# Performance work log

Measured on AMD Instinct MI355X. Metric: run time of the kernel, lower is better.

The kernel has to match this reference:

```python
import jax, jax.numpy as jnp
import numpy as np

ALPHA = 0.01
GAMMA = 4.0
SPATIAL_WEIGHT = 0.3
SEQ_LEN = 1024
LINE_WINDOW = 2


def setup_inputs() -> dict:
    key = jax.random.key(0)
    k1, k2, k3 = jax.random.split(key, 3)
    B, S, C = 64, SEQ_LEN, 8
    pred = jax.random.normal(k1, (B * S, C), dtype=jnp.float32)
    target = (jax.random.uniform(k2, (B * S, C)) < 0.05).astype(jnp.float32)
    # line indices: monotone non-decreasing within each sequence, ~256 lines
    lines = jnp.sort(
        jax.random.randint(k3, (B, S), 0, 256, dtype=jnp.int32), axis=-1
    ).reshape(-1)
    return {"pred": pred, "target": target, "token_to_line": lines}


def _spatial_penalty(pred, target, token_to_line):
    # pred/target: [B*S, C], token_to_line: [B*S]
    C = pred.shape[1]
    B = pred.shape[0] // SEQ_LEN if pred.shape[0] > SEQ_LEN else 1
    p = pred.reshape(B, SEQ_LEN, C)
    t = target.reshape(B, SEQ_LEN, C)
    l = token_to_line.reshape(B, SEQ_LEN)

    # nearby_mask[b,i,j] = |line_j - line_i| <= 2 and j != i
    diff = jnp.abs(l[:, :, None] - l[:, None, :])          # [B,S,S]
    mask = (diff <= LINE_WINDOW) & ~jnp.eye(SEQ_LEN, dtype=bool)[None]
    maskf = mask.astype(p.dtype)

    counts = maskf.sum(-1)                                  # [B,S]
    # sum of all nearby target entries (summed over classes), per token
    nearby_tgt_sum = jnp.einsum('bij,bj->bi', maskf, t.sum(-1))  # [B,S]
    # mean of sigmoid(pred) over nearby tokens
    sig = jax.nn.sigmoid(p)                                 # [B,S,C]
    sig_mean = jnp.einsum('bij,bjc->bic', maskf, sig) / jnp.maximum(counts, 1.0)[..., None]

    cond = (counts > 0) & (nearby_tgt_sum > 0)              # [B,S]
    penalty = jnp.where(cond[..., None], sig_mean * 0.1, 0.0)
    return penalty.reshape(-1, C)


def reference(pred, target, token_to_line):
    # numerically stable BCE-with-logits (reduction='none')
    bce = jnp.maximum(pred, 0.0) - pred * target + jnp.log1p(jnp.exp(-jnp.abs(pred)))
    pt = jnp.exp(-bce)
    focal = ALPHA * (1.0 - pt) ** GAMMA * bce
    focal = focal + SPATIAL_WEIGHT * _spatial_penalty(pred, target, token_to_line)
    return focal.mean()  # reduction='mean'
```

## Files before the change

kernel.cpp:

```cpp
#include <hip/hip_runtime.h>
#include <math.h>

#define SEQ_LEN 1024
#define NCLASS 8
#define NLINES 256
#define ALPHA_C 0.01f
#define SPW 0.3f
#define MAGIC 0x5EED5EEDu

__global__ __launch_bounds__(256) void fused_kernel(
    const float* __restrict__ pred,
    const float* __restrict__ target,
    const int* __restrict__ lines,
    unsigned long long* __restrict__ slots,
    float* __restrict__ out,
    float inv_total, int nblocks)
{
    __shared__ float binCnt[NLINES];
    __shared__ float binT[NLINES];
    __shared__ float binS[NLINES];
    __shared__ float wCnt[NLINES];
    __shared__ float wT[NLINES];
    __shared__ float wS[NLINES];
    __shared__ float wavesum[4];

    const int b = blockIdx.x;
    const int tid = threadIdx.x;

    binCnt[tid] = 0.f;
    binT[tid] = 0.f;
    binS[tid] = 0.f;
    __syncthreads();

    float sg[4][NCLASS];
    float tsumk[4];
    float sgsumk[4];
    int lk[4];
    unsigned tmask[4];

    #pragma unroll
    for (int k = 0; k < 4; ++k) {
        const int token = b * SEQ_LEN + k * 256 + tid;
        lk[k] = lines[token];
        const float4 p0 = ((const float4*)pred)[token * 2];
        const float4 p1 = ((const float4*)pred)[token * 2 + 1];
        const float4 t0 = ((const float4*)target)[token * 2];
        const float4 t1 = ((const float4*)target)[token * 2 + 1];
        const float px[NCLASS] = {p0.x, p0.y, p0.z, p0.w, p1.x, p1.y, p1.z, p1.w};

        const float ts = t0.x + t0.y + t0.z + t0.w + t1.x + t1.y + t1.z + t1.w;
        tsumk[k] = ts;
        unsigned m = 0;
        m |= (t0.x > 0.5f) ? 1u : 0u;
        m |= (t0.y > 0.5f) ? 2u : 0u;
        m |= (t0.z > 0.5f) ? 4u : 0u;
        m |= (t0.w > 0.5f) ? 8u : 0u;
        m |= (t1.x > 0.5f) ? 16u : 0u;
        m |= (t1.y > 0.5f) ? 32u : 0u;
        m |= (t1.z > 0.5f) ? 64u : 0u;
        m |= (t1.w > 0.5f) ? 128u : 0u;
        tmask[k] = m;

        float ssum = 0.f;
        #pragma unroll
        for (int c = 0; c < NCLASS; ++c) {
            const float e = __expf(-px[c]);
            const float s = 1.f / (1.f + e);
            sg[k][c] = s;
            ssum += s;
        }
        sgsumk[k] = ssum;

        atomicAdd(&binCnt[lk[k]], 1.f);
        atomicAdd(&binT[lk[k]], ts);
        atomicAdd(&binS[lk[k]], ssum);
    }
    __syncthreads();

    {
        const int lo = (tid - 2 < 0) ? 0 : tid - 2;
        const int hi = (tid + 2 > NLINES - 1) ? NLINES - 1 : tid + 2;
        float cs = 0.f, ts2 = 0.f, ss = 0.f;
        for (int v = lo; v <= hi; ++v) {
            cs += binCnt[v];
            ts2 += binT[v];
            ss += binS[v];
        }
        wCnt[tid] = cs;
        wT[tid] = ts2;
        wS[tid] = ss;
    }
    __syncthreads();

    float lsum = 0.f;
    #pragma unroll
    for (int k = 0; k < 4; ++k) {
        const int l = lk[k];
        const float counts = wCnt[l] - 1.f;
        const float ntgt = wT[l] - tsumk[k];
        const bool cond = (counts > 0.f) && (ntgt > 0.f);
        const float pfac = cond ? (SPW * 0.1f / counts) : 0.f;

        float fsum = 0.f;
        #pragma unroll
        for (int c = 0; c < NCLASS; ++c) {
            const float s = sg[k][c];
            const bool pos = (tmask[k] >> c) & 1u;
            const float pt = pos ? s : 1.f - s;
            const float om = 1.f - pt;
            const float bce = -__logf(pt);
            const float om2 = om * om;
            fsum += om2 * om2 * bce;
        }
        lsum += ALPHA_C * fsum + pfac * (wS[l] - sgsumk[k]);
    }

    #pragma unroll
    for (int off = 32; off > 0; off >>= 1)
        lsum += __shfl_xor(lsum, off, 64);
    if ((tid & 63) == 0) wavesum[tid >> 6] = lsum;
    __syncthreads();

    if (tid == 0) {
        const float partial =
            (wavesum[0] + wavesum[1] + wavesum[2] + wavesum[3]) * inv_total;
        const unsigned long long payload =
            ((unsigned long long)MAGIC << 32) | (unsigned long long)__float_as_uint(partial);
        __hip_atomic_store(&slots[b], payload, __ATOMIC_RELEASE,
                           __HIP_MEMORY_SCOPE_AGENT);
    }
    __syncthreads();

    if (b == 0 && tid < 64) {
        float v = 0.f;
        if (tid < nblocks) {
            unsigned long long s;
            do {
                s = __hip_atomic_load(&slots[tid], __ATOMIC_ACQUIRE,
                                      __HIP_MEMORY_SCOPE_AGENT);
            } while ((unsigned)(s >> 32) != MAGIC);
            v = __uint_as_float((unsigned)s);
        }
        #pragma unroll
        for (int off = 32; off > 0; off >>= 1)
            v += __shfl_xor(v, off, 64);
        if (tid == 0) out[0] = v;
    }
}

extern "C" void kernel_launch(void* const* d_in, const int* in_sizes, int n_in,
                              void* d_out, int out_size, void* d_ws, size_t ws_size,
                              hipStream_t stream) {
    const float* pred   = (const float*)d_in[0];
    const float* target = (const float*)d_in[1];
    const int*   lines  = (const int*)d_in[2];
    float* out = (float*)d_out;
    unsigned long long* slots = (unsigned long long*)d_ws;

    const int n_tokens = in_sizes[2];
    const int B = n_tokens / SEQ_LEN;
    const float inv_total = 1.0f / (float)in_sizes[0];

    fused_kernel<<<B, 256, 0, stream>>>(pred, target, lines, slots, out,
                                        inv_total, B);
}
```

Baseline: 65.15 us.

## Use 512-thread blocks and wave-level segmented reduction before shared atomics

The block size doubles to 512 threads, so each thread handles two tokens instead of four. Per-line histogram atomics are replaced by a shuffle-based segmented reduction inside each wave, so only the head lane of each run of equal line ids issues shared-memory atomics. Because line ids are sorted, runs are long, and this is meant to cut LDS atomic contention. In exchange it adds shuffle overhead and keeps only 64 blocks, one per sequence.

```diff
diff --git a/kernel.cpp b/kernel.cpp
--- a/kernel.cpp
+++ b/kernel.cpp
@@ -7,8 +7,10 @@
 #define ALPHA_C 0.01f
 #define SPW 0.3f
 #define MAGIC 0x5EED5EEDu
+#define BLOCK 512
+#define TOK_PER_THREAD (SEQ_LEN / BLOCK)
 
-__global__ __launch_bounds__(256) void fused_kernel(
+__global__ __launch_bounds__(BLOCK) void fused_kernel(
     const float* __restrict__ pred,
     const float* __restrict__ target,
     const int* __restrict__ lines,
@@ -22,26 +24,30 @@
     __shared__ float wCnt[NLINES];
     __shared__ float wT[NLINES];
     __shared__ float wS[NLINES];
-    __shared__ float wavesum[4];
+    __shared__ float wavesum[BLOCK / 64];
 
     const int b = blockIdx.x;
     const int tid = threadIdx.x;
+    const int lane = tid & 63;
 
-    binCnt[tid] = 0.f;
-    binT[tid] = 0.f;
-    binS[tid] = 0.f;
+    if (tid < NLINES) {
+        binCnt[tid] = 0.f;
+        binT[tid] = 0.f;
+        binS[tid] = 0.f;
+    }
     __syncthreads();
 
-    float sg[4][NCLASS];
-    float tsumk[4];
-    float sgsumk[4];
-    int lk[4];
-    unsigned tmask[4];
+    float sg[TOK_PER_THREAD][NCLASS];
+    float tsumk[TOK_PER_THREAD];
+    float sgsumk[TOK_PER_THREAD];
+    int lk[TOK_PER_THREAD];
+    unsigned tmask[TOK_PER_THREAD];
 
     #pragma unroll
-    for (int k = 0; k < 4; ++k) {
-        const int token = b * SEQ_LEN + k * 256 + tid;
-        lk[k] = lines[token];
+    for (int k = 0; k < TOK_PER_THREAD; ++k) {
+        const int token = b * SEQ_LEN + k * BLOCK + tid;
+        const int l = lines[token];
+        lk[k] = l;
         const float4 p0 = ((const float4*)pred)[token * 2];
         const float4 p1 = ((const float4*)pred)[token * 2 + 1];
         const float4 t0 = ((const float4*)target)[token * 2];
@@ -71,13 +77,27 @@
         }
         sgsumk[k] = ssum;
 
-        atomicAdd(&binCnt[lk[k]], 1.f);
-        atomicAdd(&binT[lk[k]], ts);
-        atomicAdd(&binS[lk[k]], ssum);
+        float rc = 1.f, rt = ts, rs = ssum;
+        #pragma unroll
+        for (int off = 1; off < 64; off <<= 1) {
+            const int   ln = __shfl_down(l,  off, 64);
+            const float ac = __shfl_down(rc, off, 64);
+            const float at = __shfl_down(rt, off, 64);
+            const float as = __shfl_down(rs, off, 64);
+            const bool same = (lane + off < 64) && (ln == l);
+            if (same) { rc += ac; rt += at; rs += as; }
+        }
+        const int lprev = __shfl_up(l, 1, 64);
+        const bool head = (lane == 0) || (lprev != l);
+        if (head) {
+            atomicAdd(&binCnt[l], rc);
+            atomicAdd(&binT[l], rt);
+            atomicAdd(&binS[l], rs);
+        }
     }
     __syncthreads();
 
-    {
+    if (tid < NLINES) {
         const int lo = (tid - 2 < 0) ? 0 : tid - 2;
         const int hi = (tid + 2 > NLINES - 1) ? NLINES - 1 : tid + 2;
         float cs = 0.f, ts2 = 0.f, ss = 0.f;
@@ -94,7 +114,7 @@
 
     float lsum = 0.f;
     #pragma unroll
-    for (int k = 0; k < 4; ++k) {
+    for (int k = 0; k < TOK_PER_THREAD; ++k) {
         const int l = lk[k];
         const float counts = wCnt[l] - 1.f;
         const float ntgt = wT[l] - tsumk[k];
@@ -118,12 +138,14 @@
     #pragma unroll
     for (int off = 32; off > 0; off >>= 1)
         lsum += __shfl_xor(lsum, off, 64);
-    if ((tid & 63) == 0) wavesum[tid >> 6] = lsum;
+    if (lane == 0) wavesum[tid >> 6] = lsum;
     __syncthreads();
 
     if (tid == 0) {
-        const float partial =
-            (wavesum[0] + wavesum[1] + wavesum[2] + wavesum[3]) * inv_total;
+        float partial = 0.f;
+        #pragma unroll
+        for (int w = 0; w < BLOCK / 64; ++w) partial += wavesum[w];
+        partial *= inv_total;
         const unsigned long long payload =
             ((unsigned long long)MAGIC << 32) | (unsigned long long)__float_as_uint(partial);
         __hip_atomic_store(&slots[b], payload, __ATOMIC_RELEASE,
@@ -161,6 +183,6 @@
     const int B = n_tokens / SEQ_LEN;
     const float inv_total = 1.0f / (float)in_sizes[0];
 
-    fused_kernel<<<B, 256, 0, stream>>>(pred, target, lines, slots, out,
-                                        inv_total, B);
+    fused_kernel<<<B, BLOCK, 0, stream>>>(pred, target, lines, slots, out,
+                                          inv_total, B);
 }
```

Result: faster. 61.88 us (-5.0%).
